# Kernel tuning notes

Hardware: AMD Instinct MI355X
Metric: run time of the kernel (lower is better)

Reference implementation:

```python
import jax, jax.numpy as jnp
import numpy as np

B, L, M, F = 64, 1024, 256, 256


def setup_inputs() -> dict:
    key = jax.random.key(0)
    k1, k2 = jax.random.split(key)
    patch_features = jax.random.normal(k1, (B, L, F), dtype=jnp.float32)
    queue = jax.random.normal(k2, (L, M, F), dtype=jnp.float32)
    return {"patch_features": patch_features, "queue": queue}


def reference(patch_features, queue):
    # sim[b, l, m] = <patch_features[b, l], queue[l, m]>  (batched per-location matmul)
    sim = jnp.einsum('blf,lmf->blm', patch_features, queue)
    # original takes topk(5) then keeps only index 0 == argmax over memory slots
    idx = jnp.argmax(sim, axis=-1)                      # [B, L]
    # N[b, l] = queue[l, idx[b, l]]
    N = queue[jnp.arange(queue.shape[0])[None, :], idx]  # [B, L, F]
    return N
```

## Files before the change

### kernel.cpp

```cpp
#include <hip/hip_runtime.h>

#define B_ 64
#define L_ 1024
#define M_ 256
#define F_ 256

typedef __attribute__((ext_vector_type(8))) short short8;
typedef __attribute__((ext_vector_type(16))) float f32x16;
typedef unsigned int u32;

struct Frag3 { short8 h, m, l; };

__device__ __forceinline__ u32 asu(float f) { union { float f; u32 u; } c; c.f = f; return c.u; }
__device__ __forceinline__ float asf(u32 u) { union { float f; u32 u; } c; c.u = u; return c.f; }
__device__ __forceinline__ u32 pack2(u32 lo, u32 hi) {
    return __builtin_amdgcn_perm(hi, lo, 0x07060302u);
}
__device__ __forceinline__ float4 ld4(const float* p) {
    return *reinterpret_cast<const float4*>(p);
}

__device__ __forceinline__ void async_cp16(const float* g, float* l) {
    __builtin_amdgcn_global_load_lds(
        (const __attribute__((address_space(1))) u32*)g,
        (__attribute__((address_space(3))) u32*)l,
        16, 0, 0);
}

__device__ __forceinline__ Frag3 split8(float4 a, float4 b) {
    float x[8] = {a.x, a.y, a.z, a.w, b.x, b.y, b.z, b.w};
    u32 xb[8], rb[8], sb[8];
#pragma unroll
    for (int e = 0; e < 8; ++e) {
        xb[e] = asu(x[e]);
        float hf = asf(xb[e] & 0xFFFF0000u);
        float r  = x[e] - hf;
        rb[e] = asu(r);
        float mf = asf(rb[e] & 0xFFFF0000u);
        float r2 = r - mf;
        sb[e] = asu(r2);
    }
    union { u32 w[4]; short8 s; } H, M, Lo;
#pragma unroll
    for (int d = 0; d < 4; ++d) {
        H.w[d]  = pack2(xb[2 * d], xb[2 * d + 1]);
        M.w[d]  = pack2(rb[2 * d], rb[2 * d + 1]);
        Lo.w[d] = pack2(sb[2 * d], sb[2 * d + 1]);
    }
    Frag3 f; f.h = H.s; f.m = M.s; f.l = Lo.s; return f;
}

#define MFMA6(ACC, A, Bf)                                                        \
    ACC = __builtin_amdgcn_mfma_f32_32x32x16_bf16((A).m, (Bf).m, ACC, 0, 0, 0);  \
    ACC = __builtin_amdgcn_mfma_f32_32x32x16_bf16((A).h, (Bf).l, ACC, 0, 0, 0);  \
    ACC = __builtin_amdgcn_mfma_f32_32x32x16_bf16((A).l, (Bf).h, ACC, 0, 0, 0);  \
    ACC = __builtin_amdgcn_mfma_f32_32x32x16_bf16((A).h, (Bf).m, ACC, 0, 0, 0);  \
    ACC = __builtin_amdgcn_mfma_f32_32x32x16_bf16((A).m, (Bf).h, ACC, 0, 0, 0);  \
    ACC = __builtin_amdgcn_mfma_f32_32x32x16_bf16((A).h, (Bf).h, ACC, 0, 0, 0)

__launch_bounds__(512, 2)
__global__ void mq_mfma_lds_kernel(const float* __restrict__ patch,
                                   const float* __restrict__ queue,
                                   float* __restrict__ out) {
    const int l    = blockIdx.x;
    const int t    = threadIdx.x;
    const int lane = t & 63;
    const int w    = t >> 6;
    const int bt   = w & 1;
    const int mtg  = w >> 1;
    const int r32  = lane & 31;
    const int kh   = lane >> 5;

    __shared__ __align__(16) float Ql[2][256 * 32];
    __shared__ __align__(16) float Pl[2][64 * 32];

    const int lrow = lane >> 3;
    const int lcol = lane & 7;
    const float* qsrcw = queue + ((size_t)l * M_ + w * 32 + lrow) * F_ + (lcol ^ lrow) * 4;
    const float* psrcw = patch + ((size_t)(w * 8 + lrow) * L_ + l) * F_ + (lcol ^ lrow) * 4;

#define STAGE(FT, BUF)                                                            \
    {                                                                             \
        _Pragma("unroll")                                                         \
        for (int k = 0; k < 4; ++k)                                               \
            async_cp16(qsrcw + (size_t)k * 8 * F_ + (FT) * 32,                    \
                       &Ql[BUF][(w * 4 + k) * 256]);                              \
        async_cp16(psrcw + (FT) * 32, &Pl[BUF][w * 256]);                         \
    }

    f32x16 acc0 = (f32x16)0.f, acc1 = (f32x16)0.f;

    STAGE(0, 0);

    const int s7 = r32 & 7;
    const int ra = bt * 32 + r32;
    const int rb0 = mtg * 64 + r32;
    const int rb1 = mtg * 64 + 32 + r32;

#pragma unroll 1
    for (int ft = 0; ft < 8; ++ft) {
        __builtin_amdgcn_s_barrier();
        __builtin_amdgcn_sched_barrier(0);
        if (ft < 7) {
            STAGE(ft + 1, (ft + 1) & 1);
            asm volatile("s_waitcnt vmcnt(5)" ::: "memory");
        } else {
            asm volatile("s_waitcnt vmcnt(0)" ::: "memory");
        }
        __builtin_amdgcn_sched_barrier(0);
        __builtin_amdgcn_s_barrier();
        __builtin_amdgcn_sched_barrier(0);

        const float* Qb = Ql[ft & 1];
        const float* Pb = Pl[ft & 1];
#pragma unroll
        for (int kk = 0; kk < 2; ++kk) {
            const int c0 = kk * 4 + kh * 2;
            const float4 a0 = ld4(&Pb[ra * 32 + ((c0 ^ s7) * 4)]);
            const float4 a1 = ld4(&Pb[ra * 32 + (((c0 + 1) ^ s7) * 4)]);
            const Frag3 A = split8(a0, a1);
            {
                const float4 b0 = ld4(&Qb[rb0 * 32 + ((c0 ^ s7) * 4)]);
                const float4 b1 = ld4(&Qb[rb0 * 32 + (((c0 + 1) ^ s7) * 4)]);
                const Frag3 Bf = split8(b0, b1);
                MFMA6(acc0, A, Bf);
            }
            {
                const float4 b0 = ld4(&Qb[rb1 * 32 + ((c0 ^ s7) * 4)]);
                const float4 b1 = ld4(&Qb[rb1 * 32 + (((c0 + 1) ^ s7) * 4)]);
                const Frag3 Bf = split8(b0, b1);
                MFMA6(acc1, A, Bf);
            }
        }
    }

    __syncthreads();

    float* pval = (float*)&Pl[0][0];
    int*   pidx = (int*)&Pl[0][0] + 256;
    int*   sidx = (int*)&Pl[0][0] + 512;
#pragma unroll
    for (int r = 0; r < 16; ++r) {
        float bv = acc0[r];
        int   bi = mtg * 64 + r32;
        {
            const float cv = acc1[r];
            const int   ci = mtg * 64 + 32 + r32;
            if (cv > bv) { bv = cv; bi = ci; }
        }
#pragma unroll
        for (int off = 16; off >= 1; off >>= 1) {
            const float ov = __shfl_xor(bv, off);
            const int   oi = __shfl_xor(bi, off);
            if (ov > bv || (ov == bv && oi < bi)) { bv = ov; bi = oi; }
        }
        if (r32 == 0) {
            const int b = bt * 32 + (r & 3) + 8 * (r >> 2) + 4 * kh;
            pval[mtg * 64 + b] = bv;
            pidx[mtg * 64 + b] = bi;
        }
    }
    __syncthreads();

    if (t < 64) {
        float bv = pval[t];
        int   bi = pidx[t];
#pragma unroll
        for (int g = 1; g < 4; ++g) {
            const float cv = pval[g * 64 + t];
            if (cv > bv) { bv = cv; bi = pidx[g * 64 + t]; }
        }
        sidx[t] = bi;
    }
    __syncthreads();

    const int cb = t >> 6;
    const int cc = t & 63;
#pragma unroll
    for (int b0 = 0; b0 < 64; b0 += 8) {
        const int b  = b0 + cb;
        const int mi = sidx[b];
        const float4 v = ld4(&queue[((size_t)l * M_ + mi) * F_ + cc * 4]);
        *reinterpret_cast<float4*>(&out[((size_t)b * L_ + l) * F_ + cc * 4]) = v;
    }
}

extern "C" void kernel_launch(void* const* d_in, const int* in_sizes, int n_in,
                              void* d_out, int out_size, void* d_ws, size_t ws_size,
                              hipStream_t stream) {
    const float* patch = (const float*)d_in[0];
    const float* queue = (const float*)d_in[1];
    float* out = (float*)d_out;
    mq_mfma_lds_kernel<<<dim3(L_), dim3(512), 0, stream>>>(patch, queue, out);
}
```

Measured before the change: 103.5 us.

## Process two locations per block and prefetch the second during the first

Halves the grid so each block handles locations l0 and l0+512 in sequence. The first stage of the second location's queue and patch tiles is issued during the last K-step of the first location, so that load overlaps with the argmax reduction and gather epilogue. The reduction scratch moves to the second LDS buffer so it does not clash with the in-flight prefetch into buffer 0. The intent is to hide the per-block prologue and epilogue latency, at the cost of a less flexible schedule with half as many blocks.

```diff
diff --git a/kernel.cpp b/kernel.cpp
--- a/kernel.cpp
+++ b/kernel.cpp
@@ -4,6 +4,7 @@
 #define L_ 1024
 #define M_ 256
 #define F_ 256
+#define LSTEP 512
 
 typedef __attribute__((ext_vector_type(8))) short short8;
 typedef __attribute__((ext_vector_type(16))) float f32x16;
@@ -59,10 +60,10 @@
     ACC = __builtin_amdgcn_mfma_f32_32x32x16_bf16((A).h, (Bf).h, ACC, 0, 0, 0)
 
 __launch_bounds__(512, 2)
-__global__ void mq_mfma_lds_kernel(const float* __restrict__ patch,
-                                   const float* __restrict__ queue,
-                                   float* __restrict__ out) {
-    const int l    = blockIdx.x;
+__global__ void mq_mfma_2l_kernel(const float* __restrict__ patch,
+                                  const float* __restrict__ queue,
+                                  float* __restrict__ out) {
+    const int l0   = blockIdx.x;
     const int t    = threadIdx.x;
     const int lane = t & 63;
     const int w    = t >> 6;
@@ -76,112 +77,130 @@
 
     const int lrow = lane >> 3;
     const int lcol = lane & 7;
-    const float* qsrcw = queue + ((size_t)l * M_ + w * 32 + lrow) * F_ + (lcol ^ lrow) * 4;
-    const float* psrcw = patch + ((size_t)(w * 8 + lrow) * L_ + l) * F_ + (lcol ^ lrow) * 4;
-
-#define STAGE(FT, BUF)                                                            \
+    const float* qsrcw = queue + ((size_t)l0 * M_ + w * 32 + lrow) * F_ + (lcol ^ lrow) * 4;
+    const float* psrcw = patch + ((size_t)(w * 8 + lrow) * L_ + l0) * F_ + (lcol ^ lrow) * 4;
+    const size_t QD = (size_t)LSTEP * M_ * F_;
+    const size_t PD = (size_t)LSTEP * F_;
+
+#define STAGE(QOFF, POFF, BUF)                                                    \
     {                                                                             \
         _Pragma("unroll")                                                         \
         for (int k = 0; k < 4; ++k)                                               \
-            async_cp16(qsrcw + (size_t)k * 8 * F_ + (FT) * 32,                    \
+            async_cp16(qsrcw + (size_t)k * 8 * F_ + (QOFF),                       \
                        &Ql[BUF][(w * 4 + k) * 256]);                              \
-        async_cp16(psrcw + (FT) * 32, &Pl[BUF][w * 256]);                         \
+        async_cp16(psrcw + (POFF), &Pl[BUF][w * 256]);                            \
     }
 
     f32x16 acc0 = (f32x16)0.f, acc1 = (f32x16)0.f;
 
-    STAGE(0, 0);
-
-    const int s7 = r32 & 7;
-    const int ra = bt * 32 + r32;
+    STAGE(0, 0, 0);
+
+    const int s7  = r32 & 7;
+    const int ra  = bt * 32 + r32;
     const int rb0 = mtg * 64 + r32;
     const int rb1 = mtg * 64 + 32 + r32;
 
+    float* pval = (float*)&Pl[1][0];
+    int*   pidx = (int*)&Pl[1][0] + 256;
+    int*   sidx = (int*)&Pl[1][0] + 512;
+
+#pragma unroll
+    for (int li = 0; li < 2; ++li) {
+        const size_t qo = (size_t)li * QD;
+        const size_t po = (size_t)li * PD;
+
 #pragma unroll 1
-    for (int ft = 0; ft < 8; ++ft) {
+        for (int ft = 0; ft < 8; ++ft) {
+            __builtin_amdgcn_s_barrier();
+            __builtin_amdgcn_sched_barrier(0);
+            if (ft < 7) {
+                STAGE(qo + (ft + 1) * 32, po + (ft + 1) * 32, (ft + 1) & 1);
+                asm volatile("s_waitcnt vmcnt(5)" ::: "memory");
+            } else if (li == 0) {
+                STAGE(QD, PD, 0);
+                asm volatile("s_waitcnt vmcnt(5)" ::: "memory");
+            } else {
+                asm volatile("s_waitcnt vmcnt(0)" ::: "memory");
+            }
+            __builtin_amdgcn_sched_barrier(0);
+            __builtin_amdgcn_s_barrier();
+            __builtin_amdgcn_sched_barrier(0);
+
+            const float* Qb = Ql[ft & 1];
+            const float* Pb = Pl[ft & 1];
+#pragma unroll
+            for (int kk = 0; kk < 2; ++kk) {
+                const int c0 = kk * 4 + kh * 2;
+                const float4 a0 = ld4(&Pb[ra * 32 + ((c0 ^ s7) * 4)]);
+                const float4 a1 = ld4(&Pb[ra * 32 + (((c0 + 1) ^ s7) * 4)]);
+                const Frag3 A = split8(a0, a1);
+                {
+                    const float4 b0 = ld4(&Qb[rb0 * 32 + ((c0 ^ s7) * 4)]);
+                    const float4 b1 = ld4(&Qb[rb0 * 32 + (((c0 + 1) ^ s7) * 4)]);
+                    const Frag3 Bf = split8(b0, b1);
+                    MFMA6(acc0, A, Bf);
+                }
+                {
+                    const float4 b0 = ld4(&Qb[rb1 * 32 + ((c0 ^ s7) * 4)]);
+                    const float4 b1 = ld4(&Qb[rb1 * 32 + (((c0 + 1) ^ s7) * 4)]);
+                    const Frag3 Bf = split8(b0, b1);
+                    MFMA6(acc1, A, Bf);
+                }
+            }
+        }
+
         __builtin_amdgcn_s_barrier();
-        __builtin_amdgcn_sched_barrier(0);
-        if (ft < 7) {
-            STAGE(ft + 1, (ft + 1) & 1);
-            asm volatile("s_waitcnt vmcnt(5)" ::: "memory");
-        } else {
-            asm volatile("s_waitcnt vmcnt(0)" ::: "memory");
-        }
-        __builtin_amdgcn_sched_barrier(0);
-        __builtin_amdgcn_s_barrier();
-        __builtin_amdgcn_sched_barrier(0);
-
-        const float* Qb = Ql[ft & 1];
-        const float* Pb = Pl[ft & 1];
-#pragma unroll
-        for (int kk = 0; kk < 2; ++kk) {
-            const int c0 = kk * 4 + kh * 2;
-            const float4 a0 = ld4(&Pb[ra * 32 + ((c0 ^ s7) * 4)]);
-            const float4 a1 = ld4(&Pb[ra * 32 + (((c0 + 1) ^ s7) * 4)]);
-            const Frag3 A = split8(a0, a1);
+
+#pragma unroll
+        for (int r = 0; r < 16; ++r) {
+            float bv = acc0[r];
+            int   bi = mtg * 64 + r32;
             {
-                const float4 b0 = ld4(&Qb[rb0 * 32 + ((c0 ^ s7) * 4)]);
-                const float4 b1 = ld4(&Qb[rb0 * 32 + (((c0 + 1) ^ s7) * 4)]);
-                const Frag3 Bf = split8(b0, b1);
-                MFMA6(acc0, A, Bf);
-            }
-            {
-                const float4 b0 = ld4(&Qb[rb1 * 32 + ((c0 ^ s7) * 4)]);
-                const float4 b1 = ld4(&Qb[rb1 * 32 + (((c0 + 1) ^ s7) * 4)]);
-                const Frag3 Bf = split8(b0, b1);
-                MFMA6(acc1, A, Bf);
-            }
-        }
-    }
-
-    __syncthreads();
-
-    float* pval = (float*)&Pl[0][0];
-    int*   pidx = (int*)&Pl[0][0] + 256;
-    int*   sidx = (int*)&Pl[0][0] + 512;
-#pragma unroll
-    for (int r = 0; r < 16; ++r) {
-        float bv = acc0[r];
-        int   bi = mtg * 64 + r32;
+                const float cv = acc1[r];
+                const int   ci = mtg * 64 + 32 + r32;
+                if (cv > bv) { bv = cv; bi = ci; }
+            }
+#pragma unroll
+            for (int off = 16; off >= 1; off >>= 1) {
+                const float ov = __shfl_xor(bv, off);
+                const int   oi = __shfl_xor(bi, off);
+                if (ov > bv || (ov == bv && oi < bi)) { bv = ov; bi = oi; }
+            }
+            if (r32 == 0) {
+                const int b = bt * 32 + (r & 3) + 8 * (r >> 2) + 4 * kh;
+                pval[mtg * 64 + b] = bv;
+                pidx[mtg * 64 + b] = bi;
+            }
+        }
+        __syncthreads();
+
+        if (t < 64) {
+            float bv = pval[t];
+            int   bi = pidx[t];
+#pragma unroll
+            for (int g = 1; g < 4; ++g) {
+                const float cv = pval[g * 64 + t];
+                if (cv > bv) { bv = cv; bi = pidx[g * 64 + t]; }
+            }
+            sidx[t] = bi;
+        }
+        __syncthreads();
+
         {
-            const float cv = acc1[r];
-            const int   ci = mtg * 64 + 32 + r32;
-            if (cv > bv) { bv = cv; bi = ci; }
-        }
-#pragma unroll
-        for (int off = 16; off >= 1; off >>= 1) {
-            const float ov = __shfl_xor(bv, off);
-            const int   oi = __shfl_xor(bi, off);
-            if (ov > bv || (ov == bv && oi < bi)) { bv = ov; bi = oi; }
-        }
-        if (r32 == 0) {
-            const int b = bt * 32 + (r & 3) + 8 * (r >> 2) + 4 * kh;
-            pval[mtg * 64 + b] = bv;
-            pidx[mtg * 64 + b] = bi;
-        }
-    }
-    __syncthreads();
-
-    if (t < 64) {
-        float bv = pval[t];
-        int   bi = pidx[t];
-#pragma unroll
-        for (int g = 1; g < 4; ++g) {
-            const float cv = pval[g * 64 + t];
-            if (cv > bv) { bv = cv; bi = pidx[g * 64 + t]; }
-        }
-        sidx[t] = bi;
-    }
-    __syncthreads();
-
-    const int cb = t >> 6;
-    const int cc = t & 63;
-#pragma unroll
-    for (int b0 = 0; b0 < 64; b0 += 8) {
-        const int b  = b0 + cb;
-        const int mi = sidx[b];
-        const float4 v = ld4(&queue[((size_t)l * M_ + mi) * F_ + cc * 4]);
-        *reinterpret_cast<float4*>(&out[((size_t)b * L_ + l) * F_ + cc * 4]) = v;
+            const int lcur = l0 + li * LSTEP;
+            const int cb = t >> 6;
+            const int cc = t & 63;
+#pragma unroll
+            for (int b0 = 0; b0 < 64; b0 += 8) {
+                const int b  = b0 + cb;
+                const int mi = sidx[b];
+                const float4 v = ld4(&queue[((size_t)lcur * M_ + mi) * F_ + cc * 4]);
+                *reinterpret_cast<float4*>(&out[((size_t)b * L_ + lcur) * F_ + cc * 4]) = v;
+            }
+        }
+
+        acc0 = (f32x16)0.f;
+        acc1 = (f32x16)0.f;
     }
 }
 
@@ -191,5 +210,5 @@
     const float* patch = (const float*)d_in[0];
     const float* queue = (const float*)d_in[1];
     float* out = (float*)d_out;
-    mq_mfma_lds_kernel<<<dim3(L_), dim3(512), 0, stream>>>(patch, queue, out);
-}
+    mq_mfma_2l_kernel<<<dim3(LSTEP), dim3(512), 0, stream>>>(patch, queue, out);
+}
```

Result: faster. 101.1 us (-2.3%).

## Replace double-buffered K32 staging with single-buffered K64 tiles

Applied to the files above, without the earlier changes.

Switches the F-dimension loop from eight double-buffered 32-wide stages to four single-buffered 64-wide stages, with a 16-way XOR swizzle in LDS. The loads for each stage are issued and fully awaited before compute, so global loads no longer overlap with MFMA work inside a block. In exchange there are fewer barriers and fewer loop iterations. LDS use stays about the same, so the two-blocks-per-CU occupancy is kept and other resident blocks can hide the latency.

```diff
diff --git a/kernel.cpp b/kernel.cpp
--- a/kernel.cpp
+++ b/kernel.cpp
@@ -59,7 +59,7 @@
     ACC = __builtin_amdgcn_mfma_f32_32x32x16_bf16((A).h, (Bf).h, ACC, 0, 0, 0)
 
 __launch_bounds__(512, 2)
-__global__ void mq_mfma_lds_kernel(const float* __restrict__ patch,
+__global__ void mq_mfma_k64_kernel(const float* __restrict__ patch,
                                    const float* __restrict__ queue,
                                    float* __restrict__ out) {
     const int l    = blockIdx.x;
@@ -71,63 +71,62 @@
     const int r32  = lane & 31;
     const int kh   = lane >> 5;
 
-    __shared__ __align__(16) float Ql[2][256 * 32];
-    __shared__ __align__(16) float Pl[2][64 * 32];
+    __shared__ __align__(16) float Ql[256 * 64];
+    __shared__ __align__(16) float Pl[64 * 64];
 
-    const int lrow = lane >> 3;
-    const int lcol = lane & 7;
-    const float* qsrcw = queue + ((size_t)l * M_ + w * 32 + lrow) * F_ + (lcol ^ lrow) * 4;
-    const float* psrcw = patch + ((size_t)(w * 8 + lrow) * L_ + l) * F_ + (lcol ^ lrow) * 4;
-
-#define STAGE(FT, BUF)                                                            \
-    {                                                                             \
-        _Pragma("unroll")                                                         \
-        for (int k = 0; k < 4; ++k)                                               \
-            async_cp16(qsrcw + (size_t)k * 8 * F_ + (FT) * 32,                    \
-                       &Ql[BUF][(w * 4 + k) * 256]);                              \
-        async_cp16(psrcw + (FT) * 32, &Pl[BUF][w * 256]);                         \
-    }
+    const int lrow4 = lane >> 4;
+    const int lslot = lane & 15;
 
     f32x16 acc0 = (f32x16)0.f, acc1 = (f32x16)0.f;
 
-    STAGE(0, 0);
-
-    const int s7 = r32 & 7;
-    const int ra = bt * 32 + r32;
+    const int s15 = r32 & 15;
+    const int ra  = bt * 32 + r32;
     const int rb0 = mtg * 64 + r32;
     const int rb1 = mtg * 64 + 32 + r32;
 
 #pragma unroll 1
-    for (int ft = 0; ft < 8; ++ft) {
+    for (int kt = 0; kt < 4; ++kt) {
         __builtin_amdgcn_s_barrier();
         __builtin_amdgcn_sched_barrier(0);
-        if (ft < 7) {
-            STAGE(ft + 1, (ft + 1) & 1);
-            asm volatile("s_waitcnt vmcnt(5)" ::: "memory");
-        } else {
-            asm volatile("s_waitcnt vmcnt(0)" ::: "memory");
+        {
+            const int o = kt * 64;
+#pragma unroll
+            for (int k = 0; k < 8; ++k) {
+                const int g   = w * 8 + k;
+                const int row = g * 4 + lrow4;
+                async_cp16(queue + ((size_t)l * M_ + row) * F_ + o
+                                 + ((lslot ^ (row & 15)) * 4),
+                           &Ql[(g * 4) * 64]);
+            }
+#pragma unroll
+            for (int k2 = 0; k2 < 2; ++k2) {
+                const int pg  = w * 2 + k2;
+                const int row = pg * 4 + lrow4;
+                async_cp16(patch + ((size_t)row * L_ + l) * F_ + o
+                                 + ((lslot ^ (row & 15)) * 4),
+                           &Pl[(pg * 4) * 64]);
+            }
         }
+        asm volatile("s_waitcnt vmcnt(0)" ::: "memory");
         __builtin_amdgcn_sched_barrier(0);
         __builtin_amdgcn_s_barrier();
         __builtin_amdgcn_sched_barrier(0);
 
-        const float* Qb = Ql[ft & 1];
-        const float* Pb = Pl[ft & 1];
 #pragma unroll
-        for (int kk = 0; kk < 2; ++kk) {
+        for (int kk = 0; kk < 4; ++kk) {
             const int c0 = kk * 4 + kh * 2;
-            const float4 a0 = ld4(&Pb[ra * 32 + ((c0 ^ s7) * 4)]);
-            const float4 a1 = ld4(&Pb[ra * 32 + (((c0 + 1) ^ s7) * 4)]);
+            const float4 a0 = ld4(&Pl[ra * 64 + ((c0 ^ s15) * 4)]);
+            const float4 a1 = ld4(&Pl[ra * 64 + (((c0 + 1) ^ s15) * 4)]);
             const Frag3 A = split8(a0, a1);
             {
-                const float4 b0 = ld4(&Qb[rb0 * 32 + ((c0 ^ s7) * 4)]);
-                const float4 b1 = ld4(&Qb[rb0 * 32 + (((c0 + 1) ^ s7) * 4)]);
+                const float4 b0 = ld4(&Ql[rb0 * 64 + ((c0 ^ s15) * 4)]);
+                const float4 b1 = ld4(&Ql[rb0 * 64 + (((c0 + 1) ^ s15) * 4)]);
                 const Frag3 Bf = split8(b0, b1);
                 MFMA6(acc0, A, Bf);
             }
             {
-                const float4 b0 = ld4(&Qb[rb1 * 32 + ((c0 ^ s7) * 4)]);
-                const float4 b1 = ld4(&Qb[rb1 * 32 + (((c0 + 1) ^ s7) * 4)]);
+                const float4 b0 = ld4(&Ql[rb1 * 64 + ((c0 ^ s15) * 4)]);
+                const float4 b1 = ld4(&Ql[rb1 * 64 + (((c0 + 1) ^ s15) * 4)]);
                 const Frag3 Bf = split8(b0, b1);
                 MFMA6(acc1, A, Bf);
             }
@@ -136,9 +135,9 @@
 
     __syncthreads();
 
-    float* pval = (float*)&Pl[0][0];
-    int*   pidx = (int*)&Pl[0][0] + 256;
-    int*   sidx = (int*)&Pl[0][0] + 512;
+    float* pval = (float*)&Pl[0];
+    int*   pidx = (int*)&Pl[0] + 256;
+    int*   sidx = (int*)&Pl[0] + 512;
 #pragma unroll
     for (int r = 0; r < 16; ++r) {
         float bv = acc0[r];
@@ -191,5 +190,5 @@
     const float* patch = (const float*)d_in[0];
     const float* queue = (const float*)d_in[1];
     float* out = (float*)d_out;
-    mq_mfma_lds_kernel<<<dim3(L_), dim3(512), 0, stream>>>(patch, queue, out);
+    mq_mfma_k64_kernel<<<dim3(L_), dim3(512), 0, stream>>>(patch, queue, out);
 }
```

Result: slower. 106.4 us (+2.7%).
